# Kernel tuning notes

Hardware: AMD Instinct MI355X
Metric: run time of the kernel (lower is better)

## Reference

```python
import jax, jax.numpy as jnp
import numpy as np

DIM = 1024
INTER = 2048
N_EXPERTS = 8
TOP_K = 2
ROUTE_SCALE = 1.0


def setup_inputs() -> dict:
    key = jax.random.key(0)
    ks = jax.random.split(key, 4)
    x = jax.random.normal(ks[0], (4, 2048, DIM), dtype=jnp.float32)
    # Gate weight matches nn.Parameter(torch.randn(n_experts, dim))
    Wg = jax.random.normal(ks[1], (N_EXPERTS, DIM), dtype=jnp.float32)
    W1 = jax.random.normal(ks[2], (N_EXPERTS, DIM, INTER), dtype=jnp.float32) * (1.0 / np.sqrt(DIM))
    b1 = jnp.zeros((N_EXPERTS, INTER), dtype=jnp.float32)
    W2 = jax.random.normal(ks[3], (N_EXPERTS, INTER, DIM), dtype=jnp.float32) * (1.0 / np.sqrt(INTER))
    b2 = jnp.zeros((N_EXPERTS, DIM), dtype=jnp.float32)
    return {"x": x, "Wg": Wg, "W1": W1, "b1": b1, "W2": W2, "b2": b2}


def reference(x, Wg, W1, b1, W2, b2):
    # Flatten tokens: [T, D]
    xt = x.reshape(-1, DIM)
    T = xt.shape[0]

    # --- Gate: sigmoid scores, top-k, normalized weights ---
    scores = jax.nn.sigmoid(xt @ Wg.T)                       # [T, E]
    top_w, top_idx = jax.lax.top_k(scores, TOP_K)            # [T, K]
    top_w = top_w / jnp.sum(top_w, axis=-1, keepdims=True)
    top_w = top_w * ROUTE_SCALE

    # Sparse combine weights [T, E] (top_k indices are distinct per token)
    cw = jnp.zeros((T, N_EXPERTS), dtype=xt.dtype)
    cw = cw.at[jnp.arange(T)[:, None], top_idx].set(top_w)

    # --- Experts: dense per-expert MLP, weighted combine ---
    # (dropout is identity in eval mode)
    h = jax.nn.relu(jnp.einsum('td,edh->eth', xt, W1) + b1[:, None, :])   # [E, T, H]
    eo = jnp.einsum('eth,ehd->etd', h, W2) + b2[:, None, :]               # [E, T, D]
    y = jnp.einsum('etd,te->td', eo, cw)                                  # [T, D]
    return y
```

## Files before the change

### kernel.cpp

```cpp
#include <hip/hip_runtime.h>
#include <stdint.h>

#define DIM   1024
#define INTER 2048
#define NEXP  8

typedef _Float16 f16;
typedef __attribute__((ext_vector_type(4))) _Float16 f16x4;
typedef __attribute__((ext_vector_type(8))) _Float16 f16x8;
typedef __attribute__((ext_vector_type(4))) float    f32x4;

static __device__ __forceinline__ void gload16(const void* gsrc, void* lds) {
    __builtin_amdgcn_global_load_lds(
        (const __attribute__((address_space(1))) uint32_t*)gsrc,
        (__attribute__((address_space(3))) uint32_t*)lds,
        16, 0, 0);
}

__global__ void gate_convert_kernel(const float* __restrict__ x, const float* __restrict__ Wg,
                                    f16* __restrict__ xh, float* __restrict__ gw,
                                    int* __restrict__ gidx, int T) {
    const int tok  = (int)((blockIdx.x * (size_t)blockDim.x + threadIdx.x) >> 6);
    const int lane = threadIdx.x & 63;
    if (tok >= T) return;
    const float4* xr  = (const float4*)(x + (size_t)tok * DIM);
    f16*          xhr = xh + (size_t)tok * DIM;
    float s[NEXP];
    #pragma unroll
    for (int e = 0; e < NEXP; ++e) s[e] = 0.f;
    #pragma unroll
    for (int it = 0; it < 4; ++it) {
        int i = it * 64 + lane;
        float4 xv = xr[i];
        f16x4 hv = { (f16)xv.x, (f16)xv.y, (f16)xv.z, (f16)xv.w };
        *(f16x4*)(xhr + i * 4) = hv;
        #pragma unroll
        for (int e = 0; e < NEXP; ++e) {
            float4 wv = ((const float4*)(Wg + e * DIM))[i];
            s[e] += xv.x * wv.x + xv.y * wv.y + xv.z * wv.z + xv.w * wv.w;
        }
    }
    #pragma unroll
    for (int e = 0; e < NEXP; ++e) {
        #pragma unroll
        for (int off = 32; off > 0; off >>= 1) s[e] += __shfl_xor(s[e], off);
    }
    if (lane == 0) {
        float sc[NEXP];
        #pragma unroll
        for (int e = 0; e < NEXP; ++e) sc[e] = 1.f / (1.f + expf(-s[e]));
        int i0 = 0;
        #pragma unroll
        for (int e = 1; e < NEXP; ++e) if (sc[e] > sc[i0]) i0 = e;
        int i1 = -1;
        #pragma unroll
        for (int e = 0; e < NEXP; ++e) if (e != i0 && (i1 < 0 || sc[e] > sc[i1])) i1 = e;
        float w0 = sc[i0], w1 = sc[i1];
        float inv = 1.f / (w0 + w1);
        gw[2 * tok + 0] = w0 * inv;
        gw[2 * tok + 1] = w1 * inv;
        gidx[2 * tok + 0] = i0;
        gidx[2 * tok + 1] = i1;
    }
}

__global__ void transpose_conv_kernel(const float* __restrict__ W, f16* __restrict__ Wt, int K, int N) {
    __shared__ f16 tile[64][65];
    const int e  = blockIdx.z;
    const int kb = blockIdx.y * 64;
    const int nb = blockIdx.x * 64;
    const int tx = threadIdx.x & 63;
    const int ty = threadIdx.x >> 6;
    const float* We  = W  + (size_t)e * K * N;
    f16*         Wte = Wt + (size_t)e * K * N;
    #pragma unroll
    for (int i = 0; i < 16; ++i) {
        int k = ty + i * 4;
        tile[k][tx] = (f16)We[(size_t)(kb + k) * N + nb + tx];
    }
    __syncthreads();
    #pragma unroll
    for (int i = 0; i < 16; ++i) {
        int n = ty + i * 4;
        Wte[(size_t)(nb + n) * K + kb + tx] = tile[tx][n];
    }
}

__global__ __launch_bounds__(1024)
void route_kernel(const int* __restrict__ gidx, int* __restrict__ offsets,
                  int* __restrict__ tor, int* __restrict__ ros, int T) {
    const int tid  = threadIdx.x;
    const int lane = tid & 63;
    const int wv   = tid >> 6;
    const int NE   = 2 * T;
    __shared__ int wc[16][NEXP];
    __shared__ int rb[NEXP];

    int c[NEXP];
    #pragma unroll
    for (int e = 0; e < NEXP; ++e) c[e] = 0;
    for (int i = tid; i < NE; i += 1024) {
        int g = gidx[i];
        #pragma unroll
        for (int e = 0; e < NEXP; ++e) c[e] += (g == e) ? 1 : 0;
    }
    #pragma unroll
    for (int e = 0; e < NEXP; ++e) {
        #pragma unroll
        for (int off = 32; off > 0; off >>= 1) c[e] += __shfl_xor(c[e], off);
    }
    if (lane == 0) {
        #pragma unroll
        for (int e = 0; e < NEXP; ++e) wc[wv][e] = c[e];
    }
    __syncthreads();
    if (tid == 0) {
        int acc = 0;
        for (int e = 0; e < NEXP; ++e) {
            int t = 0;
            for (int w2 = 0; w2 < 16; ++w2) t += wc[w2][e];
            offsets[e] = acc;
            rb[e] = acc;
            acc += t;
        }
        offsets[NEXP] = acc;
    }
    __syncthreads();

    for (int base = 0; base < NE; base += 1024) {
        int i = base + tid;
        int g = gidx[i];
        int myrank = 0;
        #pragma unroll
        for (int e = 0; e < NEXP; ++e) {
            unsigned long long m = __ballot(g == e);
            if (g == e) myrank = __popcll(m & ((1ull << lane) - 1ull));
            if (lane == 0) wc[wv][e] = __popcll(m);
        }
        __syncthreads();
        int pre = 0;
        for (int w2 = 0; w2 < wv; ++w2) pre += wc[w2][g];
        int pos = rb[g] + pre + myrank;
        tor[pos] = i >> 1;
        ros[i]   = pos;
        __syncthreads();
        if (tid < NEXP) {
            int t = 0;
            for (int w2 = 0; w2 < 16; ++w2) t += wc[w2][tid];
            rb[tid] += t;
        }
        __syncthreads();
    }
}

template<int KD, int ND, bool RELU, bool GATHER, int RT>
__global__ __launch_bounds__(256)
void moe_gemm_kernel(const f16* __restrict__ Abase, const f16* __restrict__ Bt,
                     const float* __restrict__ bias, const int* __restrict__ offsets,
                     const int* __restrict__ tok, f16* __restrict__ Cout) {
    constexpr int NT  = ND / 128;
    constexpr int NT2 = NT / 2;
    constexpr int RT4 = RT / 4;
    const int bid = blockIdx.x;
    const int xcd = bid & 7;
    const int j   = bid >> 3;
    const int nt  = (j % NT2) * 2 + (xcd & 1);
    const int rt  = ((j / NT2) % RT4) * 4 + (xcd >> 1);
    const int e   = j / (NT2 * RT4);

    const int rowBeg = offsets[e];
    const int rowEnd = offsets[e + 1];
    const int row0   = rowBeg + rt * 128;
    if (row0 >= rowEnd) return;
    const int n0   = nt * 128;
    const int tid  = threadIdx.x;
    const int lane = tid & 63;
    const int wid  = tid >> 6;
    const int wr   = (wid >> 1) * 64;
    const int wc   = (wid & 1) * 64;

    __shared__ __align__(16) f16 As[128 * 64];
    __shared__ __align__(16) f16 Bs[128 * 64];

    const f16* Bte = Bt + (size_t)e * ND * KD;

    int aOff[4], bOff[4], ldsOff[4];
    #pragma unroll
    for (int i = 0; i < 4; ++i) {
        int c  = i * 256 + tid;
        int r  = c >> 3;
        int kc = (c & 7) ^ (r & 7);
        ldsOff[i] = c * 8;
        int gr = row0 + r;
        if (gr >= rowEnd) gr = rowEnd - 1;
        int ar = GATHER ? tok[gr] : gr;
        aOff[i] = ar * KD + kc * 8;
        bOff[i] = (n0 + r) * KD + kc * 8;
    }

    f32x4 acc[4][4] = {};

    const int rb    = lane & 15;
    const int jbase = lane >> 4;

    constexpr int nK = KD / 64;
    for (int kt = 0; kt < nK; ++kt) {
        const int k0 = kt * 64;
        #pragma unroll
        for (int i = 0; i < 4; ++i)
            gload16(Abase + (size_t)(aOff[i] + k0), &As[ldsOff[i]]);
        #pragma unroll
        for (int i = 0; i < 4; ++i)
            gload16(Bte + (size_t)(bOff[i] + k0), &Bs[ldsOff[i]]);
        __syncthreads();

        #pragma unroll
        for (int ks = 0; ks < 2; ++ks) {
            const int sl = (((ks * 4 + jbase) ^ (rb & 7))) * 8;
            f16x8 af[4], bfr[4];
            #pragma unroll
            for (int m = 0; m < 4; ++m)
                af[m] = *(const f16x8*)&As[(wr + m * 16 + rb) * 64 + sl];
            #pragma unroll
            for (int n = 0; n < 4; ++n)
                bfr[n] = *(const f16x8*)&Bs[(wc + n * 16 + rb) * 64 + sl];
            #pragma unroll
            for (int m = 0; m < 4; ++m)
                #pragma unroll
                for (int n = 0; n < 4; ++n)
                    acc[m][n] = __builtin_amdgcn_mfma_f32_16x16x32_f16(af[m], bfr[n], acc[m][n], 0, 0, 0);
        }

        __syncthreads();
    }

    const int rowsValid = rowEnd - row0;
    #pragma unroll
    for (int m = 0; m < 4; ++m) {
        #pragma unroll
        for (int n = 0; n < 4; ++n) {
            #pragma unroll
            for (int j2 = 0; j2 < 4; ++j2) {
                int rl  = wr + m * 16 + ((lane >> 4) << 2) + j2;
                int col = n0 + wc + n * 16 + (lane & 15);
                if (rl < rowsValid) {
                    float v = acc[m][n][j2] + bias[e * ND + col];
                    if (RELU) v = fmaxf(v, 0.f);
                    Cout[(size_t)(row0 + rl) * ND + col] = (f16)v;
                }
            }
        }
    }
}

__global__ void combine_kernel(const f16* __restrict__ eo, const int* __restrict__ ros,
                               const float* __restrict__ gw, float* __restrict__ y, int T) {
    int gid = blockIdx.x * 256 + threadIdx.x;
    int t   = gid >> 7;
    if (t >= T) return;
    int c0 = (gid & 127) * 8;
    int r0 = ros[2 * t], r1 = ros[2 * t + 1];
    float w0 = gw[2 * t], w1 = gw[2 * t + 1];
    f16x8 v0 = *(const f16x8*)(eo + (size_t)r0 * DIM + c0);
    f16x8 v1 = *(const f16x8*)(eo + (size_t)r1 * DIM + c0);
    f32x4 o0, o1;
    #pragma unroll
    for (int j = 0; j < 4; ++j) o0[j] = w0 * (float)v0[j] + w1 * (float)v1[j];
    #pragma unroll
    for (int j = 0; j < 4; ++j) o1[j] = w0 * (float)v0[4 + j] + w1 * (float)v1[4 + j];
    *(f32x4*)(y + (size_t)t * DIM + c0)     = o0;
    *(f32x4*)(y + (size_t)t * DIM + c0 + 4) = o1;
}

extern "C" void kernel_launch(void* const* d_in, const int* in_sizes, int n_in,
                              void* d_out, int out_size, void* d_ws, size_t ws_size,
                              hipStream_t stream) {
    const float* x  = (const float*)d_in[0];
    const float* Wg = (const float*)d_in[1];
    const float* W1 = (const float*)d_in[2];
    const float* b1 = (const float*)d_in[3];
    const float* W2 = (const float*)d_in[4];
    const float* b2 = (const float*)d_in[5];
    float* y = (float*)d_out;
    const int T = in_sizes[0] / DIM;

    char* ws = (char*)d_ws;
    size_t off = 0;
    auto alloc = [&](size_t bytes) -> char* {
        char* p = ws + off;
        off += (bytes + 255) & ~(size_t)255;
        return p;
    };
    f16* xh   = (f16*)alloc((size_t)T * DIM * 2);
    f16* w1t  = (f16*)alloc((size_t)NEXP * DIM * INTER * 2);
    f16* w2t  = (f16*)alloc((size_t)NEXP * DIM * INTER * 2);
    f16* h    = (f16*)alloc((size_t)2 * T * INTER * 2);
    f16* eo   = (f16*)alloc((size_t)2 * T * DIM * 2);
    float* gw = (float*)alloc((size_t)T * 2 * 4);
    int* gidx = (int*)alloc((size_t)T * 2 * 4);
    int* ros  = (int*)alloc((size_t)T * 2 * 4);
    int* tor  = (int*)alloc((size_t)2 * T * 4);
    int* offsets = (int*)alloc(64 * 4);

    gate_convert_kernel<<<T / 4, 256, 0, stream>>>(x, Wg, xh, gw, gidx, T);
    transpose_conv_kernel<<<dim3(INTER / 64, DIM / 64, NEXP), 256, 0, stream>>>(W1, w1t, DIM, INTER);
    transpose_conv_kernel<<<dim3(DIM / 64, INTER / 64, NEXP), 256, 0, stream>>>(W2, w2t, INTER, DIM);
    route_kernel<<<1, 1024, 0, stream>>>(gidx, offsets, tor, ros, T);
    moe_gemm_kernel<DIM, INTER, true, true, 64>
        <<<dim3(((INTER / 128) / 2) * (64 / 4) * NEXP * 8), 256, 0, stream>>>(xh, w1t, b1, offsets, tor, h);
    moe_gemm_kernel<INTER, DIM, false, false, 64>
        <<<dim3(((DIM / 128) / 2) * (64 / 4) * NEXP * 8), 256, 0, stream>>>(h, w2t, b2, offsets, tor, eo);
    combine_kernel<<<(T * DIM / 8 + 255) / 256, 256, 0, stream>>>(eo, ros, gw, y, T);
}
```

Before: 329.8 us.

## Use compact tile list for MoE GEMM grids and vectorize weight transpose

The route kernel now builds a compact list of (expert, row-start) tiles, and both MoE GEMMs launch one block per listed tile instead of a fixed 64 row-tiles per expert that mostly exit early. This cuts the empty-block launch overhead, since the launch shrinks from 8192 to about 2176 blocks for GEMM1. Separately, the weight transpose/convert kernel uses float4 loads and 16-byte f16x8 stores, with a padded LDS tile. The risk is the fixed TIMAX=136 bound: it holds for T=8192 with 2 experts per token (at most 128+8 tiles) but is not checked.

```diff
diff --git a/kernel.cpp b/kernel.cpp
--- a/kernel.cpp
+++ b/kernel.cpp
@@ -4,8 +4,10 @@
 #define DIM   1024
 #define INTER 2048
 #define NEXP  8
+#define TIMAX 136
 
 typedef _Float16 f16;
+typedef __attribute__((ext_vector_type(2))) _Float16 f16x2;
 typedef __attribute__((ext_vector_type(4))) _Float16 f16x4;
 typedef __attribute__((ext_vector_type(8))) _Float16 f16x8;
 typedef __attribute__((ext_vector_type(4))) float    f32x4;
@@ -65,30 +67,41 @@
 }
 
 __global__ void transpose_conv_kernel(const float* __restrict__ W, f16* __restrict__ Wt, int K, int N) {
-    __shared__ f16 tile[64][65];
+    __shared__ f16 tile[64][66];
     const int e  = blockIdx.z;
     const int kb = blockIdx.y * 64;
     const int nb = blockIdx.x * 64;
-    const int tx = threadIdx.x & 63;
-    const int ty = threadIdx.x >> 6;
+    const int t  = threadIdx.x;
     const float* We  = W  + (size_t)e * K * N;
     f16*         Wte = Wt + (size_t)e * K * N;
-    #pragma unroll
-    for (int i = 0; i < 16; ++i) {
-        int k = ty + i * 4;
-        tile[k][tx] = (f16)We[(size_t)(kb + k) * N + nb + tx];
+    const int kl = t >> 4;
+    const int nq = t & 15;
+    #pragma unroll
+    for (int pass = 0; pass < 4; ++pass) {
+        int k = pass * 16 + kl;
+        float4 v = *(const float4*)&We[(size_t)(kb + k) * N + nb + nq * 4];
+        f16x2 lo = { (f16)v.x, (f16)v.y };
+        f16x2 hi = { (f16)v.z, (f16)v.w };
+        *(f16x2*)&tile[k][nq * 4]     = lo;
+        *(f16x2*)&tile[k][nq * 4 + 2] = hi;
     }
     __syncthreads();
-    #pragma unroll
-    for (int i = 0; i < 16; ++i) {
-        int n = ty + i * 4;
-        Wte[(size_t)(nb + n) * K + kb + tx] = tile[tx][n];
-    }
+    const int n  = t >> 2;
+    const int kq = t & 3;
+    f16x8 o0, o1;
+    #pragma unroll
+    for (int i = 0; i < 8; ++i) o0[i] = tile[kq * 16 + i][n];
+    #pragma unroll
+    for (int i = 0; i < 8; ++i) o1[i] = tile[kq * 16 + 8 + i][n];
+    f16* dst = &Wte[(size_t)(nb + n) * K + kb + kq * 16];
+    *(f16x8*)dst       = o0;
+    *(f16x8*)(dst + 8) = o1;
 }
 
 __global__ __launch_bounds__(1024)
 void route_kernel(const int* __restrict__ gidx, int* __restrict__ offsets,
-                  int* __restrict__ tor, int* __restrict__ ros, int T) {
+                  int* __restrict__ tor, int* __restrict__ ros,
+                  int* __restrict__ tileE, int* __restrict__ tileR0, int T) {
     const int tid  = threadIdx.x;
     const int lane = tid & 63;
     const int wv   = tid >> 6;
@@ -124,6 +137,14 @@
             acc += t;
         }
         offsets[NEXP] = acc;
+        int nt = 0;
+        for (int e = 0; e < NEXP; ++e)
+            for (int r0 = offsets[e]; r0 < offsets[e + 1]; r0 += 128) {
+                tileE[nt]  = e;
+                tileR0[nt] = r0;
+                ++nt;
+            }
+        for (; nt < TIMAX; ++nt) { tileE[nt] = -1; tileR0[nt] = 0; }
     }
     __syncthreads();
 
@@ -153,25 +174,25 @@
     }
 }
 
-template<int KD, int ND, bool RELU, bool GATHER, int RT>
+template<int KD, int ND, bool RELU, bool GATHER>
 __global__ __launch_bounds__(256)
 void moe_gemm_kernel(const f16* __restrict__ Abase, const f16* __restrict__ Bt,
                      const float* __restrict__ bias, const int* __restrict__ offsets,
-                     const int* __restrict__ tok, f16* __restrict__ Cout) {
+                     const int* __restrict__ tok, const int* __restrict__ tileE,
+                     const int* __restrict__ tileR0, f16* __restrict__ Cout) {
     constexpr int NT  = ND / 128;
     constexpr int NT2 = NT / 2;
-    constexpr int RT4 = RT / 4;
     const int bid = blockIdx.x;
     const int xcd = bid & 7;
     const int j   = bid >> 3;
     const int nt  = (j % NT2) * 2 + (xcd & 1);
-    const int rt  = ((j / NT2) % RT4) * 4 + (xcd >> 1);
-    const int e   = j / (NT2 * RT4);
-
-    const int rowBeg = offsets[e];
+    const int tih = j / NT2;
+    const int ti  = tih * 4 + (xcd >> 1);
+
+    const int e = tileE[ti];
+    if (e < 0) return;
+    const int row0   = tileR0[ti];
     const int rowEnd = offsets[e + 1];
-    const int row0   = rowBeg + rt * 128;
-    if (row0 >= rowEnd) return;
     const int n0   = nt * 128;
     const int tid  = threadIdx.x;
     const int lane = tid & 63;
@@ -301,14 +322,16 @@
     int* ros  = (int*)alloc((size_t)T * 2 * 4);
     int* tor  = (int*)alloc((size_t)2 * T * 4);
     int* offsets = (int*)alloc(64 * 4);
+    int* tileE   = (int*)alloc(TIMAX * 4);
+    int* tileR0  = (int*)alloc(TIMAX * 4);
 
     gate_convert_kernel<<<T / 4, 256, 0, stream>>>(x, Wg, xh, gw, gidx, T);
     transpose_conv_kernel<<<dim3(INTER / 64, DIM / 64, NEXP), 256, 0, stream>>>(W1, w1t, DIM, INTER);
     transpose_conv_kernel<<<dim3(DIM / 64, INTER / 64, NEXP), 256, 0, stream>>>(W2, w2t, INTER, DIM);
-    route_kernel<<<1, 1024, 0, stream>>>(gidx, offsets, tor, ros, T);
-    moe_gemm_kernel<DIM, INTER, true, true, 64>
-        <<<dim3(((INTER / 128) / 2) * (64 / 4) * NEXP * 8), 256, 0, stream>>>(xh, w1t, b1, offsets, tor, h);
-    moe_gemm_kernel<INTER, DIM, false, false, 64>
-        <<<dim3(((DIM / 128) / 2) * (64 / 4) * NEXP * 8), 256, 0, stream>>>(h, w2t, b2, offsets, tor, eo);
+    route_kernel<<<1, 1024, 0, stream>>>(gidx, offsets, tor, ros, tileE, tileR0, T);
+    moe_gemm_kernel<DIM, INTER, true, true>
+        <<<dim3((TIMAX / 4) * ((INTER / 128) / 2) * 8), 256, 0, stream>>>(xh, w1t, b1, offsets, tor, tileE, tileR0, h);
+    moe_gemm_kernel<INTER, DIM, false, false>
+        <<<dim3((TIMAX / 4) * ((DIM / 128) / 2) * 8), 256, 0, stream>>>(h, w2t, b2, offsets, tor, tileE, tileR0, eo);
     combine_kernel<<<(T * DIM / 8 + 255) / 256, 256, 0, stream>>>(eo, ros, gw, y, T);
 }
```

Measured after the change: 331.8 us. About the same (+0.6%).
